# Kernel optimization log

Hardware: AMD Instinct MI355X
Metric: run time of the kernel (lower is better)

The kernel has to match this reference:

```python
import jax, jax.numpy as jnp
import numpy as np

B, S, D, H = 4, 2048, 1024, 16
HD = D // H  # head_dim = 64


def setup_inputs() -> dict:
    key = jax.random.key(0)
    kx, kq, kk, kv, ko = jax.random.split(key, 5)
    scale = 1.0 / np.sqrt(D)
    return {
        "x": jax.random.normal(kx, (B, S, D), dtype=jnp.float32),
        "Wq": jax.random.normal(kq, (D, D), dtype=jnp.float32) * scale,
        "Wk": jax.random.normal(kk, (D, D), dtype=jnp.float32) * scale,
        "Wv": jax.random.normal(kv, (D, D), dtype=jnp.float32) * scale,
        "Wo": jax.random.normal(ko, (D, D), dtype=jnp.float32) * scale,
    }


def reference(x, Wq, Wk, Wv, Wo):
    b, s, d = x.shape
    # torch nn.Linear: y = x @ W.T
    q = (x @ Wq.T).reshape(b, s, H, HD).transpose(0, 2, 1, 3)  # [B,H,S,hd]
    k = (x @ Wk.T).reshape(b, s, H, HD).transpose(0, 2, 1, 3)
    v = (x @ Wv.T).reshape(b, s, H, HD).transpose(0, 2, 1, 3)
    attn = jnp.einsum("bhqd,bhkd->bhqk", q, k) / np.sqrt(HD)  # [B,H,S,S]
    attn = jax.nn.softmax(attn, axis=-1)
    out = jnp.einsum("bhqk,bhkd->bhqd", attn, v)  # [B,H,S,hd]
    per_head = out.transpose(0, 2, 1, 3)  # [B,S,H,hd]
    combined = per_head.reshape(b, s, d)
    projected = combined @ Wo.T
    return projected, per_head
```

## Files before the change

kernel.cpp:

```cpp
#include <hip/hip_runtime.h>
#include <hip/hip_bf16.h>

#define BB 4
#define SS 2048
#define DD 1024
#define HH 16
#define HDD 64
#define MM (BB*SS)

using bf16x8  = __attribute__((ext_vector_type(8))) short;
using f32x4   = __attribute__((ext_vector_type(4))) float;
using f32x16  = __attribute__((ext_vector_type(16))) float;
using ushort8 = __attribute__((ext_vector_type(8))) unsigned short;
using ushort4v= __attribute__((ext_vector_type(4))) unsigned short;
using uint4v  = __attribute__((ext_vector_type(4))) unsigned int;

#if __has_builtin(__builtin_amdgcn_exp2f)
#define EXP2(x) __builtin_amdgcn_exp2f(x)
#else
#define EXP2(x) exp2f(x)
#endif

__device__ __forceinline__ unsigned short f2bf(float x) {
    unsigned u = __builtin_bit_cast(unsigned, x);
    u += 0x7FFFu + ((u >> 16) & 1u);
    return (unsigned short)(u >> 16);
}

__device__ __forceinline__ unsigned int cvtpk(float lo, float hi) {
    unsigned int r;
    asm("v_cvt_pk_bf16_f32 %0, %1, %2" : "=v"(r) : "v"(lo), "v"(hi));
    return r;
}

#define PSWAP(a, b) asm("v_permlane32_swap_b32 %0, %1" : "+v"(a), "+v"(b))

__device__ __forceinline__ void load_lds16(const void* g, void* l) {
    __builtin_amdgcn_global_load_lds(
        (const __attribute__((address_space(1))) void*)g,
        (__attribute__((address_space(3))) void*)l, 16, 0, 0);
}

__global__ __launch_bounds__(256) void cvt_all(const float* __restrict__ x,
                                               const float* __restrict__ wq,
                                               const float* __restrict__ wk,
                                               const float* __restrict__ wv,
                                               const float* __restrict__ wo,
                                               unsigned short* __restrict__ ox,
                                               unsigned short* __restrict__ oq,
                                               unsigned short* __restrict__ ok,
                                               unsigned short* __restrict__ ov,
                                               unsigned short* __restrict__ oo) {
    const int z = blockIdx.y;
    const float* src;
    unsigned short* dst;
    float scale = 1.0f;
    size_t base;
    if (z < 8)       { src = x;  dst = ox; base = (size_t)z * 512 * 2048; }
    else if (z == 8) { src = wq; dst = oq; base = 0; scale = 0.18033688011112042f; }
    else if (z == 9) { src = wk; dst = ok; base = 0; }
    else if (z == 10){ src = wv; dst = ov; base = 0; }
    else             { src = wo; dst = oo; base = 0; }
    size_t i = base + ((size_t)blockIdx.x * 256 + threadIdx.x) * 8;
    float4 a = *(const float4*)(src + i);
    float4 b = *(const float4*)(src + i + 4);
    ushort8 r;
    r[0] = f2bf(a.x*scale); r[1] = f2bf(a.y*scale); r[2] = f2bf(a.z*scale); r[3] = f2bf(a.w*scale);
    r[4] = f2bf(b.x*scale); r[5] = f2bf(b.y*scale); r[6] = f2bf(b.z*scale); r[7] = f2bf(b.w*scale);
    *(ushort8*)(dst + i) = r;
}

template<int LAYOUT>
__device__ __forceinline__ void gemm_body(const unsigned short* __restrict__ A,
                                          const unsigned short* __restrict__ W,
                                          void* __restrict__ Cout,
                                          unsigned short* As, unsigned short* Bs) {
    const int t    = threadIdx.x;
    const int lane = t & 63, wid = t >> 6;
    const int wr   = wid >> 1, wc = wid & 1;
    const int lrow = lane & 15, lkg = lane >> 4;
    const int lid  = blockIdx.y * 8 + blockIdx.x;
    const int ord  = (lid & 7) * 64 + (lid >> 3);
    const int row0 = (ord >> 3) * 128, col0 = (ord & 7) * 128;

    f32x4 acc[4][4];
    #pragma unroll
    for (int m = 0; m < 4; ++m)
        #pragma unroll
        for (int n = 0; n < 4; ++n) acc[m][n] = (f32x4){0.f, 0.f, 0.f, 0.f};

    const int c0 = t, c1 = t + 256;
    const unsigned short* Ag0 = A + (size_t)(row0 + (c0 >> 2)) * DD + (c0 & 3) * 8;
    const unsigned short* Ag1 = A + (size_t)(row0 + (c1 >> 2)) * DD + (c1 & 3) * 8;
    const unsigned short* Wg0 = W + (size_t)(col0 + (c0 >> 2)) * DD + (c0 & 3) * 8;
    const unsigned short* Wg1 = W + (size_t)(col0 + (c1 >> 2)) * DD + (c1 & 3) * 8;

    auto stage = [&](int buf, int k0) {
        load_lds16(Ag0 + k0, &As[buf*128*32 + c0 * 8]);
        load_lds16(Ag1 + k0, &As[buf*128*32 + c1 * 8]);
        load_lds16(Wg0 + k0, &Bs[buf*128*32 + c0 * 8]);
        load_lds16(Wg1 + k0, &Bs[buf*128*32 + c1 * 8]);
    };

    stage(0, 0);
    __syncthreads();
    for (int kt = 0; kt < DD / 32; ++kt) {
        const int cur = kt & 1;
        if (kt + 1 < DD / 32) stage(cur ^ 1, (kt + 1) * 32);
        bf16x8 af[4], bfr[4];
        #pragma unroll
        for (int m = 0; m < 4; ++m)
            af[m] = *(const bf16x8*)&As[cur*128*32 + (wr*64 + m*16 + lrow) * 32 + lkg*8];
        #pragma unroll
        for (int n = 0; n < 4; ++n)
            bfr[n] = *(const bf16x8*)&Bs[cur*128*32 + (wc*64 + n*16 + lrow) * 32 + lkg*8];
        __builtin_amdgcn_s_setprio(1);
        #pragma unroll
        for (int m = 0; m < 4; ++m)
            #pragma unroll
            for (int n = 0; n < 4; ++n)
                acc[m][n] = __builtin_amdgcn_mfma_f32_16x16x32_bf16(af[m], bfr[n], acc[m][n], 0, 0, 0);
        __builtin_amdgcn_s_setprio(0);
        __syncthreads();
    }

    #pragma unroll
    for (int m = 0; m < 4; ++m) {
        #pragma unroll
        for (int n = 0; n < 4; ++n) {
            if (LAYOUT == 2) {
                int gm0 = row0 + wr*64 + m*16 + lkg*4;
                int gn  = col0 + wc*64 + n*16 + lrow;
                int b_ = gm0 >> 11, s0 = gm0 & 2047;
                int h_ = gn >> 6,  hd = gn & 63;
                ushort4v hv;
                hv[0] = f2bf(acc[m][n][0]); hv[1] = f2bf(acc[m][n][1]);
                hv[2] = f2bf(acc[m][n][2]); hv[3] = f2bf(acc[m][n][3]);
                *(ushort4v*)&((unsigned short*)Cout)[(((size_t)b_*HH + h_)*HDD + hd)*SS + s0] = hv;
            } else {
                #pragma unroll
                for (int j = 0; j < 4; ++j) {
                    int gm = row0 + wr*64 + m*16 + lkg*4 + j;
                    int gn = col0 + wc*64 + n*16 + lrow;
                    float v = acc[m][n][j];
                    if (LAYOUT == 1) {
                        int b_ = gm >> 11, s_ = gm & 2047;
                        int h_ = gn >> 6,  hd = gn & 63;
                        ((unsigned short*)Cout)[(((size_t)b_*HH + h_)*SS + s_)*HDD + hd] = f2bf(v);
                    } else {
                        ((float*)Cout)[(size_t)gm * DD + gn] = v;
                    }
                }
            }
        }
    }
}

__global__ __launch_bounds__(256) void gemm_qkv(const unsigned short* __restrict__ A,
                                                const unsigned short* __restrict__ Wq,
                                                const unsigned short* __restrict__ Wk,
                                                const unsigned short* __restrict__ Wv,
                                                unsigned short* __restrict__ Q,
                                                unsigned short* __restrict__ K,
                                                unsigned short* __restrict__ V) {
    __shared__ unsigned short As[2*128*32];
    __shared__ unsigned short Bs[2*128*32];
    const int z = blockIdx.z;
    if (z == 2)      gemm_body<2>(A, Wv, V, As, Bs);
    else if (z == 1) gemm_body<1>(A, Wk, K, As, Bs);
    else             gemm_body<1>(A, Wq, Q, As, Bs);
}

__global__ __launch_bounds__(256) void gemm_proj(const unsigned short* __restrict__ A,
                                                 const unsigned short* __restrict__ W,
                                                 float* __restrict__ C) {
    __shared__ unsigned short As[2*128*32];
    __shared__ unsigned short Bs[2*128*32];
    gemm_body<0>(A, W, C, As, Bs);
}

__global__ __launch_bounds__(256, 2) void flash_mfma7(const unsigned short* __restrict__ Qg,
                                                      const unsigned short* __restrict__ Kg,
                                                      const unsigned short* __restrict__ Vtg,
                                                      float* __restrict__ outf,
                                                      unsigned short* __restrict__ outb) {
    __shared__ unsigned short Ks[2][64*64];
    __shared__ unsigned short Vs[2][64*64];
    const int t   = threadIdx.x, lane = t & 63, wid = t >> 6;
    const int l31 = lane & 31;
    const int hi  = lane >> 5;
    const int lid = blockIdx.y * 8 + blockIdx.x;
    const int ord = (lid & 7) * 64 + (lid >> 3);
    const int bh  = ord >> 3, b_ = bh >> 4, h_ = bh & 15;
    const int qA  = (ord & 7) * 256 + wid * 32;

    const unsigned short* Qb = Qg  + (size_t)bh * SS * HDD;
    const unsigned short* Kb = Kg  + (size_t)bh * SS * HDD;
    const unsigned short* Vb = Vtg + (size_t)bh * HDD * SS;

    bf16x8 qfA[4], qfB[4];
    #pragma unroll
    for (int ks = 0; ks < 4; ++ks) {
        qfA[ks] = *(const bf16x8*)&Qb[(size_t)(qA + l31) * HDD + ks*16 + hi*8];
        qfB[ks] = *(const bf16x8*)&Qb[(size_t)(qA + 128 + l31) * HDD + ks*16 + hi*8];
    }

    f32x16 osA0, osA1, osB0, osB1, sumA, sumB, z;
    #pragma unroll
    for (int r = 0; r < 16; ++r) {
        osA0[r] = 0.f; osA1[r] = 0.f; osB0[r] = 0.f; osB1[r] = 0.f;
        sumA[r] = 0.f; sumB[r] = 0.f; z[r] = 0.f;
    }

    bf16x8 onesf;
    #pragma unroll
    for (int e = 0; e < 8; ++e) onesf[e] = (short)0x3F80;

    const int c0 = t, c1 = t + 256;
    const unsigned sb0 = ((unsigned)(c0 << 4)) ^ ((((unsigned)c0 >> 3) & 7u) << 4);
    const unsigned sb1 = ((unsigned)(c1 << 4)) ^ ((((unsigned)c1 >> 3) & 7u) << 4);
    const unsigned xs  = ((unsigned)(l31 & 7)) << 4;

    bf16x8 kr0, kr1, vr0, vr1;
    kr0 = *(const bf16x8*)&Kb[8*c0];
    kr1 = *(const bf16x8*)&Kb[8*c1];
    vr0 = *(const bf16x8*)&Vb[(size_t)(c0 >> 3) * SS + (c0 & 7) * 8];
    vr1 = *(const bf16x8*)&Vb[(size_t)(c1 >> 3) * SS + (c1 & 7) * 8];
    *(bf16x8*)((char*)&Ks[0][0] + sb0) = kr0;
    *(bf16x8*)((char*)&Ks[0][0] + sb1) = kr1;
    *(bf16x8*)((char*)&Vs[0][0] + sb0) = vr0;
    *(bf16x8*)((char*)&Vs[0][0] + sb1) = vr1;
    __syncthreads();

    for (int kt = 0; kt < SS/64; ++kt) {
        const int cur = kt & 1;
        if (kt + 1 < SS/64) {
            kr0 = *(const bf16x8*)&Kb[(size_t)(kt+1)*4096 + 8*c0];
            kr1 = *(const bf16x8*)&Kb[(size_t)(kt+1)*4096 + 8*c1];
            vr0 = *(const bf16x8*)&Vb[(size_t)(c0 >> 3) * SS + (kt+1)*64 + (c0 & 7) * 8];
            vr1 = *(const bf16x8*)&Vb[(size_t)(c1 >> 3) * SS + (kt+1)*64 + (c1 & 7) * 8];
        }
        const char* Kc = (const char*)&Ks[cur][0];
        const char* Vc = (const char*)&Vs[cur][0];

        f32x16 saA0, saA1, saB0, saB1;
        __builtin_amdgcn_s_setprio(1);
        #pragma unroll
        for (int ks = 0; ks < 4; ++ks) {
            const unsigned cb = ks*32 + hi*16;
            bf16x8 kf0 = *(const bf16x8*)(Kc + (((unsigned)(l31*128)      + cb) ^ xs));
            bf16x8 kf1 = *(const bf16x8*)(Kc + (((unsigned)((32+l31)*128) + cb) ^ xs));
            if (ks == 0) {
                saA0 = __builtin_amdgcn_mfma_f32_32x32x16_bf16(kf0, qfA[0], z, 0, 0, 0);
                saA1 = __builtin_amdgcn_mfma_f32_32x32x16_bf16(kf1, qfA[0], z, 0, 0, 0);
                saB0 = __builtin_amdgcn_mfma_f32_32x32x16_bf16(kf0, qfB[0], z, 0, 0, 0);
                saB1 = __builtin_amdgcn_mfma_f32_32x32x16_bf16(kf1, qfB[0], z, 0, 0, 0);
            } else {
                saA0 = __builtin_amdgcn_mfma_f32_32x32x16_bf16(kf0, qfA[ks], saA0, 0, 0, 0);
                saA1 = __builtin_amdgcn_mfma_f32_32x32x16_bf16(kf1, qfA[ks], saA1, 0, 0, 0);
                saB0 = __builtin_amdgcn_mfma_f32_32x32x16_bf16(kf0, qfB[ks], saB0, 0, 0, 0);
                saB1 = __builtin_amdgcn_mfma_f32_32x32x16_bf16(kf1, qfB[ks], saB1, 0, 0, 0);
            }
        }
        __builtin_amdgcn_s_setprio(0);

        unsigned int pkA0[4][2], pkA1[4][2], pkB0[4][2], pkB1[4][2];
        #pragma unroll
        for (int a = 0; a < 4; ++a) {
            #pragma unroll
            for (int h = 0; h < 2; ++h) {
                pkA0[a][h] = cvtpk(EXP2(saA0[4*a + 2*h]), EXP2(saA0[4*a + 2*h + 1]));
                pkA1[a][h] = cvtpk(EXP2(saA1[4*a + 2*h]), EXP2(saA1[4*a + 2*h + 1]));
                pkB0[a][h] = cvtpk(EXP2(saB0[4*a + 2*h]), EXP2(saB0[4*a + 2*h + 1]));
                pkB1[a][h] = cvtpk(EXP2(saB1[4*a + 2*h]), EXP2(saB1[4*a + 2*h + 1]));
            }
        }

        __builtin_amdgcn_s_setprio(1);
        #pragma unroll
        for (int ksg = 0; ksg < 4; ++ksg) {
            const int ks2 = (ksg & 1) * 2;
            unsigned int a0, a1, a2, a3, b0, b1, b2, b3;
            if ((ksg >> 1) == 0) {
                a0 = pkA0[ks2][0]; a2 = pkA0[ks2+1][0]; a1 = pkA0[ks2][1]; a3 = pkA0[ks2+1][1];
                b0 = pkB0[ks2][0]; b2 = pkB0[ks2+1][0]; b1 = pkB0[ks2][1]; b3 = pkB0[ks2+1][1];
            } else {
                a0 = pkA1[ks2][0]; a2 = pkA1[ks2+1][0]; a1 = pkA1[ks2][1]; a3 = pkA1[ks2+1][1];
                b0 = pkB1[ks2][0]; b2 = pkB1[ks2+1][0]; b1 = pkB1[ks2][1]; b3 = pkB1[ks2+1][1];
            }
            PSWAP(a0, a2); PSWAP(a1, a3);
            PSWAP(b0, b2); PSWAP(b1, b3);
            uint4v wa = {a0, a1, a2, a3};
            uint4v wb = {b0, b1, b2, b3};
            bf16x8 pfA = __builtin_bit_cast(bf16x8, wa);
            bf16x8 pfB = __builtin_bit_cast(bf16x8, wb);
            const unsigned cb = ksg*32 + hi*16;
            bf16x8 vf0 = *(const bf16x8*)(Vc + (((unsigned)(l31*128)      + cb) ^ xs));
            bf16x8 vf1 = *(const bf16x8*)(Vc + (((unsigned)((32+l31)*128) + cb) ^ xs));
            osA0 = __builtin_amdgcn_mfma_f32_32x32x16_bf16(vf0, pfA, osA0, 0, 0, 0);
            osA1 = __builtin_amdgcn_mfma_f32_32x32x16_bf16(vf1, pfA, osA1, 0, 0, 0);
            osB0 = __builtin_amdgcn_mfma_f32_32x32x16_bf16(vf0, pfB, osB0, 0, 0, 0);
            osB1 = __builtin_amdgcn_mfma_f32_32x32x16_bf16(vf1, pfB, osB1, 0, 0, 0);
            sumA = __builtin_amdgcn_mfma_f32_32x32x16_bf16(onesf, pfA, sumA, 0, 0, 0);
            sumB = __builtin_amdgcn_mfma_f32_32x32x16_bf16(onesf, pfB, sumB, 0, 0, 0);
        }
        __builtin_amdgcn_s_setprio(0);

        if (kt + 1 < SS/64) {
            char* Kn = (char*)&Ks[cur ^ 1][0];
            char* Vn = (char*)&Vs[cur ^ 1][0];
            *(bf16x8*)(Kn + sb0) = kr0;
            *(bf16x8*)(Kn + sb1) = kr1;
            *(bf16x8*)(Vn + sb0) = vr0;
            *(bf16x8*)(Vn + sb1) = vr1;
        }
        __syncthreads();
    }

    #pragma unroll
    for (int g = 0; g < 2; ++g) {
        const float invl = 1.0f / (g == 0 ? sumA[0] : sumB[0]);
        const int   s_   = qA + (g ? 128 : 0) + l31;
        float*          po = outf + (((size_t)b_ * SS + s_) * HH + h_) * HDD;
        unsigned short* pb = outb + (((size_t)b_ * SS + s_) * HH + h_) * HDD;
        #pragma unroll
        for (int a = 0; a < 4; ++a) {
            {
                const f32x16& o = g == 0 ? osA0 : osB0;
                const int d0 = 8*a + 4*hi;
                float4 v; v.x = o[4*a+0]*invl; v.y = o[4*a+1]*invl;
                          v.z = o[4*a+2]*invl; v.w = o[4*a+3]*invl;
                *(float4*)&po[d0] = v;
                ushort4v hv; hv[0]=f2bf(v.x); hv[1]=f2bf(v.y); hv[2]=f2bf(v.z); hv[3]=f2bf(v.w);
                *(ushort4v*)&pb[d0] = hv;
            }
            {
                const f32x16& o = g == 0 ? osA1 : osB1;
                const int d0 = 32 + 8*a + 4*hi;
                float4 v; v.x = o[4*a+0]*invl; v.y = o[4*a+1]*invl;
                          v.z = o[4*a+2]*invl; v.w = o[4*a+3]*invl;
                *(float4*)&po[d0] = v;
                ushort4v hv; hv[0]=f2bf(v.x); hv[1]=f2bf(v.y); hv[2]=f2bf(v.z); hv[3]=f2bf(v.w);
                *(ushort4v*)&pb[d0] = hv;
            }
        }
    }
}

extern "C" void kernel_launch(void* const* d_in, const int* in_sizes, int n_in,
                              void* d_out, int out_size, void* d_ws, size_t ws_size,
                              hipStream_t stream) {
    const float* x  = (const float*)d_in[0];
    const float* Wq = (const float*)d_in[1];
    const float* Wk = (const float*)d_in[2];
    const float* Wv = (const float*)d_in[3];
    const float* Wo = (const float*)d_in[4];
    float* out      = (float*)d_out;
    float* per_head = out + (size_t)MM * DD;

    unsigned short* ws   = (unsigned short*)d_ws;
    const size_t NE = (size_t)MM * DD;
    unsigned short* Qbf  = ws;
    unsigned short* Kbf  = Qbf + NE;
    unsigned short* Vbf  = Kbf + NE;
    unsigned short* xbf  = Vbf + NE;
    unsigned short* wqbf = xbf + NE;
    unsigned short* wkbf = wqbf + (size_t)DD * DD;
    unsigned short* wvbf = wkbf + (size_t)DD * DD;
    unsigned short* wobf = wvbf + (size_t)DD * DD;
    unsigned short* cbf  = wobf + (size_t)DD * DD;

    cvt_all<<<dim3(512, 12), 256, 0, stream>>>(x, Wq, Wk, Wv, Wo,
                                               xbf, wqbf, wkbf, wvbf, wobf);

    gemm_qkv<<<dim3(DD / 128, MM / 128, 3), 256, 0, stream>>>(xbf, wqbf, wkbf, wvbf,
                                                              Qbf, Kbf, Vbf);

    flash_mfma7<<<dim3(8, BB * HH), 256, 0, stream>>>(Qbf, Kbf, Vbf, per_head, cbf);

    gemm_proj<<<dim3(DD / 128, MM / 128), 256, 0, stream>>>(cbf, wobf, out);
}
```

Measured before the change: 191.1 us.

## Replace QKV GEMM with 256x256-tile 8-wave kernel using direct LDS loads

Replaces the 128x128-tile, 4-wave QKV projection GEMM with a 512-thread kernel that computes 256x256 tiles. It treats Wq/Wk/Wv as one concatenated 3072-row weight matrix, relying on them being contiguous in the workspace. Operands are staged through direct global-to-LDS loads into a 4-slot ring with an XOR swizzle, and each wave computes a 128x64 sub-tile with a register-blocked MFMA schedule. The aim is more data reuse per byte loaded, fewer LDS bank conflicts and better latency hiding. The cost is higher register and LDS pressure, and only 384 blocks are launched, which may limit occupancy.

After: 196.8 us. 1.03x slower.

```diff
diff --git a/kernel.cpp b/kernel.cpp
--- a/kernel.cpp
+++ b/kernel.cpp
@@ -70,11 +70,157 @@
     *(ushort8*)(dst + i) = r;
 }
 
-template<int LAYOUT>
-__device__ __forceinline__ void gemm_body(const unsigned short* __restrict__ A,
-                                          const unsigned short* __restrict__ W,
-                                          void* __restrict__ Cout,
-                                          unsigned short* As, unsigned short* Bs) {
+__global__ __launch_bounds__(512, 2) void gemm8_qkv(const unsigned short* __restrict__ A,
+                                                    const unsigned short* __restrict__ W,
+                                                    unsigned short* __restrict__ Q,
+                                                    unsigned short* __restrict__ K,
+                                                    unsigned short* __restrict__ V) {
+    __shared__ unsigned short Asl[4 * 8192];
+    __shared__ unsigned short Bsl[4 * 8192];
+
+    const int tid  = threadIdx.x;
+    const int lane = tid & 63, wid = tid >> 6;
+    const int lrow = lane & 15, lkg = lane >> 4;
+    const int wm   = wid >> 2;
+    const int wn   = wid & 3;
+
+    const int lid    = blockIdx.y * 12 + blockIdx.x;
+    const int ord    = (lid & 7) * 48 + (lid >> 3);
+    const int rowBlk = ord / 12, colBlk = ord % 12;
+    const int row0   = rowBlk * 256;
+    const int col0g  = colBlk * 256;
+
+    const int sA   = tid ^ (((tid >> 5) & 1) << 1);
+    const int srow = sA >> 3;
+    const int scol = (sA & 7) * 8;
+
+    auto stageT = [&](int tt) {
+        #pragma unroll
+        for (int h = 0; h < 2; ++h) {
+            const int slot = (2 * tt + h) & 3;
+            #pragma unroll
+            for (int j = 0; j < 2; ++j) {
+                const int r = h * 128 + j * 64 + srow;
+                load_lds16(A + (size_t)(row0 + r) * DD + tt * 64 + scol,
+                           (char*)Asl + slot * 16384 + (j * 512 + tid) * 16);
+                load_lds16(W + (size_t)(col0g + r) * DD + tt * 64 + scol,
+                           (char*)Bsl + slot * 16384 + (j * 512 + tid) * 16);
+            }
+        }
+    };
+
+    f32x4 acc[8][4];
+    #pragma unroll
+    for (int m = 0; m < 8; ++m)
+        #pragma unroll
+        for (int n = 0; n < 4; ++n) acc[m][n] = (f32x4){0.f, 0.f, 0.f, 0.f};
+
+    stageT(0);
+    stageT(1);
+    __syncthreads();
+
+    const unsigned kcol0 = (unsigned)(lkg * 16);
+    for (int tt = 0; tt < 16; ++tt) {
+        const unsigned baseA = (unsigned)(((2 * tt + wm) & 3) * 16384);
+        const unsigned baseB = (unsigned)(((2 * tt + (wn >> 1)) & 3) * 16384);
+
+        auto ldA = [&](int m, int ks) -> bf16x8 {
+            const int r = m * 16 + lrow;
+            const unsigned off = baseA + (unsigned)(r * 128)
+                + (((unsigned)(ks * 64) + kcol0) ^ ((((unsigned)lrow >> 2) & 1u) << 5));
+            return *(const bf16x8*)((const char*)Asl + off);
+        };
+        auto ldB = [&](int n, int ks) -> bf16x8 {
+            const int c = (wn & 1) * 64 + n * 16 + lrow;
+            const unsigned off = baseB + (unsigned)(c * 128)
+                + (((unsigned)(ks * 64) + kcol0) ^ ((((unsigned)lrow >> 2) & 1u) << 5));
+            return *(const bf16x8*)((const char*)Bsl + off);
+        };
+
+        bf16x8 af[4][2], b0[2][2], b1[2][2];
+
+        #pragma unroll
+        for (int mi = 0; mi < 4; ++mi) { af[mi][0] = ldA(mi, 0); af[mi][1] = ldA(mi, 1); }
+        #pragma unroll
+        for (int ni = 0; ni < 2; ++ni) { b0[ni][0] = ldB(ni, 0); b0[ni][1] = ldB(ni, 1); }
+        __builtin_amdgcn_s_setprio(1);
+        #pragma unroll
+        for (int mi = 0; mi < 4; ++mi)
+            #pragma unroll
+            for (int ni = 0; ni < 2; ++ni)
+                #pragma unroll
+                for (int ks = 0; ks < 2; ++ks)
+                    acc[mi][ni] = __builtin_amdgcn_mfma_f32_16x16x32_bf16(af[mi][ks], b0[ni][ks], acc[mi][ni], 0, 0, 0);
+        __builtin_amdgcn_s_setprio(0);
+
+        #pragma unroll
+        for (int ni = 0; ni < 2; ++ni) { b1[ni][0] = ldB(2 + ni, 0); b1[ni][1] = ldB(2 + ni, 1); }
+        __builtin_amdgcn_s_setprio(1);
+        #pragma unroll
+        for (int mi = 0; mi < 4; ++mi)
+            #pragma unroll
+            for (int ni = 0; ni < 2; ++ni)
+                #pragma unroll
+                for (int ks = 0; ks < 2; ++ks)
+                    acc[mi][2 + ni] = __builtin_amdgcn_mfma_f32_16x16x32_bf16(af[mi][ks], b1[ni][ks], acc[mi][2 + ni], 0, 0, 0);
+        __builtin_amdgcn_s_setprio(0);
+
+        #pragma unroll
+        for (int mi = 0; mi < 4; ++mi) { af[mi][0] = ldA(4 + mi, 0); af[mi][1] = ldA(4 + mi, 1); }
+        __builtin_amdgcn_s_setprio(1);
+        #pragma unroll
+        for (int mi = 0; mi < 4; ++mi)
+            #pragma unroll
+            for (int ni = 0; ni < 2; ++ni)
+                #pragma unroll
+                for (int ks = 0; ks < 2; ++ks)
+                    acc[4 + mi][2 + ni] = __builtin_amdgcn_mfma_f32_16x16x32_bf16(af[mi][ks], b1[ni][ks], acc[4 + mi][2 + ni], 0, 0, 0);
+        __builtin_amdgcn_s_setprio(0);
+
+        __builtin_amdgcn_s_setprio(1);
+        #pragma unroll
+        for (int mi = 0; mi < 4; ++mi)
+            #pragma unroll
+            for (int ni = 0; ni < 2; ++ni)
+                #pragma unroll
+                for (int ks = 0; ks < 2; ++ks)
+                    acc[4 + mi][ni] = __builtin_amdgcn_mfma_f32_16x16x32_bf16(af[mi][ks], b0[ni][ks], acc[4 + mi][ni], 0, 0, 0);
+        __builtin_amdgcn_s_setprio(0);
+
+        __syncthreads();
+        if (tt + 2 < 16) stageT(tt + 2);
+    }
+
+    const int zt = colBlk >> 2;
+    const int lcol0 = (colBlk & 3) * 256;
+    unsigned short* dstQK = (zt == 1) ? K : Q;
+    #pragma unroll
+    for (int m = 0; m < 8; ++m) {
+        #pragma unroll
+        for (int n = 0; n < 4; ++n) {
+            const int gm0 = row0 + wm * 128 + m * 16 + lkg * 4;
+            const int gn  = lcol0 + wn * 64 + n * 16 + lrow;
+            const int b_ = gm0 >> 11, s0 = gm0 & 2047;
+            const int h_ = gn >> 6,  hd = gn & 63;
+            if (zt == 2) {
+                ushort4v hv;
+                hv[0] = f2bf(acc[m][n][0]); hv[1] = f2bf(acc[m][n][1]);
+                hv[2] = f2bf(acc[m][n][2]); hv[3] = f2bf(acc[m][n][3]);
+                *(ushort4v*)&V[(((size_t)b_ * HH + h_) * HDD + hd) * SS + s0] = hv;
+            } else {
+                #pragma unroll
+                for (int j = 0; j < 4; ++j)
+                    dstQK[(((size_t)b_ * HH + h_) * SS + (s0 + j)) * HDD + hd] = f2bf(acc[m][n][j]);
+            }
+        }
+    }
+}
+
+__global__ __launch_bounds__(256) void gemm_proj(const unsigned short* __restrict__ A,
+                                                 const unsigned short* __restrict__ W,
+                                                 float* __restrict__ C) {
+    __shared__ unsigned short As[2*128*32];
+    __shared__ unsigned short Bs[2*128*32];
     const int t    = threadIdx.x;
     const int lane = t & 63, wid = t >> 6;
     const int wr   = wid >> 1, wc = wid & 1;
@@ -125,58 +271,15 @@
     }
 
     #pragma unroll
-    for (int m = 0; m < 4; ++m) {
-        #pragma unroll
-        for (int n = 0; n < 4; ++n) {
-            if (LAYOUT == 2) {
-                int gm0 = row0 + wr*64 + m*16 + lkg*4;
-                int gn  = col0 + wc*64 + n*16 + lrow;
-                int b_ = gm0 >> 11, s0 = gm0 & 2047;
-                int h_ = gn >> 6,  hd = gn & 63;
-                ushort4v hv;
-                hv[0] = f2bf(acc[m][n][0]); hv[1] = f2bf(acc[m][n][1]);
-                hv[2] = f2bf(acc[m][n][2]); hv[3] = f2bf(acc[m][n][3]);
-                *(ushort4v*)&((unsigned short*)Cout)[(((size_t)b_*HH + h_)*HDD + hd)*SS + s0] = hv;
-            } else {
-                #pragma unroll
-                for (int j = 0; j < 4; ++j) {
-                    int gm = row0 + wr*64 + m*16 + lkg*4 + j;
-                    int gn = col0 + wc*64 + n*16 + lrow;
-                    float v = acc[m][n][j];
-                    if (LAYOUT == 1) {
-                        int b_ = gm >> 11, s_ = gm & 2047;
-                        int h_ = gn >> 6,  hd = gn & 63;
-                        ((unsigned short*)Cout)[(((size_t)b_*HH + h_)*SS + s_)*HDD + hd] = f2bf(v);
-                    } else {
-                        ((float*)Cout)[(size_t)gm * DD + gn] = v;
-                    }
-                }
-            }
-        }
-    }
-}
-
-__global__ __launch_bounds__(256) void gemm_qkv(const unsigned short* __restrict__ A,
-                                                const unsigned short* __restrict__ Wq,
-                                                const unsigned short* __restrict__ Wk,
-                                                const unsigned short* __restrict__ Wv,
-                                                unsigned short* __restrict__ Q,
-                                                unsigned short* __restrict__ K,
-                                                unsigned short* __restrict__ V) {
-    __shared__ unsigned short As[2*128*32];
-    __shared__ unsigned short Bs[2*128*32];
-    const int z = blockIdx.z;
-    if (z == 2)      gemm_body<2>(A, Wv, V, As, Bs);
-    else if (z == 1) gemm_body<1>(A, Wk, K, As, Bs);
-    else             gemm_body<1>(A, Wq, Q, As, Bs);
-}
-
-__global__ __launch_bounds__(256) void gemm_proj(const unsigned short* __restrict__ A,
-                                                 const unsigned short* __restrict__ W,
-                                                 float* __restrict__ C) {
-    __shared__ unsigned short As[2*128*32];
-    __shared__ unsigned short Bs[2*128*32];
-    gemm_body<0>(A, W, C, As, Bs);
+    for (int m = 0; m < 4; ++m)
+        #pragma unroll
+        for (int n = 0; n < 4; ++n)
+            #pragma unroll
+            for (int j = 0; j < 4; ++j) {
+                int gm = row0 + wr*64 + m*16 + lkg*4 + j;
+                int gn = col0 + wc*64 + n*16 + lrow;
+                C[(size_t)gm * DD + gn] = acc[m][n][j];
+            }
 }
 
 __global__ __launch_bounds__(256, 2) void flash_mfma7(const unsigned short* __restrict__ Qg,
@@ -373,8 +476,7 @@
     cvt_all<<<dim3(512, 12), 256, 0, stream>>>(x, Wq, Wk, Wv, Wo,
                                                xbf, wqbf, wkbf, wvbf, wobf);
 
-    gemm_qkv<<<dim3(DD / 128, MM / 128, 3), 256, 0, stream>>>(xbf, wqbf, wkbf, wvbf,
-                                                              Qbf, Kbf, Vbf);
+    gemm8_qkv<<<dim3(12, 32), 512, 0, stream>>>(xbf, wqbf, Qbf, Kbf, Vbf);
 
     flash_mfma7<<<dim3(8, BB * HH), 256, 0, stream>>>(Qbf, Kbf, Vbf, per_head, cbf);
 
```
